# Kernel optimization log

Hardware: AMD Instinct MI355X
Metric: run time of the kernel (lower is better)

## Reference

```python
import jax, jax.numpy as jnp
import numpy as np

N, NFEAT, NHID, NCLASS, NHEADS = 4096, 512, 64, 128, 8
ALPHA = 0.2
NEG = -9e15


def leaky(x):
    return jnp.where(x > 0, x, ALPHA * x)


def setup_inputs() -> dict:
    key = jax.random.key(0)
    k = jax.random.split(key, 6)
    x = jax.random.normal(k[0], (N, NFEAT), dtype=jnp.float32)
    adj = jax.random.randint(k[1], (N, N), 0, 2, dtype=jnp.int32)
    # per-head params (xavier-ish scale)
    W = jax.random.normal(k[2], (NHEADS, NFEAT, NHID), dtype=jnp.float32) * (1.414 * (2.0 / (NFEAT + NHID)) ** 0.5)
    a = jax.random.normal(k[3], (NHEADS, 2 * NHID), dtype=jnp.float32) * (1.414 * (2.0 / (2 * NHID + 1)) ** 0.5)
    W_out = jax.random.normal(k[4], (NHEADS * NHID, NCLASS), dtype=jnp.float32) * (1.414 * (2.0 / (NHEADS * NHID + NCLASS)) ** 0.5)
    a_out = jax.random.normal(k[5], (2 * NCLASS,), dtype=jnp.float32) * (1.414 * (2.0 / (2 * NCLASS + 1)) ** 0.5)
    return {"x": x, "adj": adj, "W": W, "a": a, "W_out": W_out, "a_out": a_out}


def _gat_layer_multihead(x, adj_mask, W, a):
    # x: [N,F_in], W: [H,F_in,F_out], a: [H,2*F_out]
    h = jnp.einsum('nf,hfo->hno', x, W)           # [H,N,F_out]
    Fo = W.shape[-1]
    a1, a2 = a[:, :Fo], a[:, Fo:]                  # [H,F_out] each
    fi = jnp.einsum('hno,ho->hn', h, a1)           # score contribution of node i
    fj = jnp.einsum('hno,ho->hn', h, a2)
    e = leaky(fi[:, :, None] + fj[:, None, :])     # [H,N,N] == leakyrelu(a . [h_i||h_j])
    e = jnp.where(adj_mask[None], e, NEG)
    att = jax.nn.softmax(e, axis=-1)
    return jnp.einsum('hij,hjo->hio', att, h)      # [H,N,F_out]


def reference(x, adj, W, a, W_out, a_out):
    adj_mask = adj > 0
    # multi-head hidden layer, concat heads (dropout is identity in eval mode)
    hp = _gat_layer_multihead(x, adj_mask, W, a)            # [H,N,NHID]
    xcat = jnp.transpose(hp, (1, 0, 2)).reshape(N, NHEADS * NHID)
    # output attention layer (single head)
    out = _gat_layer_multihead(xcat, adj_mask, W_out[None], a_out[None])[0]  # [N,NCLASS]
    out = jax.nn.elu(out)
    return jax.nn.log_softmax(out, axis=1)
```

## Files before the change

### kernel.cpp

```cpp
#include <hip/hip_runtime.h>
#include <hip/hip_bf16.h>

#define NNODE 4096

typedef __attribute__((ext_vector_type(8))) short bf16x8;
typedef __attribute__((ext_vector_type(4))) float f32x4;
typedef __attribute__((ext_vector_type(8))) unsigned short us8;

__device__ __forceinline__ float leaky(float x) { return x > 0.0f ? x : 0.2f * x; }

__device__ __forceinline__ unsigned short f2bf(float x) {
  __hip_bfloat16 b = __float2bfloat16(x);
  return __builtin_bit_cast(unsigned short, b);
}

__global__ __launch_bounds__(256) void packadj(
    const int* __restrict__ adj, unsigned long long* __restrict__ mask) {
  size_t wid = (size_t)blockIdx.x * 4 + (threadIdx.x >> 6);
  int v = adj[wid * 64 + (threadIdx.x & 63)];
  unsigned long long b = __ballot(v != 0);
  if ((threadIdx.x & 63) == 0) mask[wid] = b;
}

__global__ __launch_bounds__(256) void gemm64(
    const float* __restrict__ A, const float* __restrict__ B, float* __restrict__ C,
    int M, int K, int Nfull) {
  __shared__ float Ast[64][68];
  __shared__ float Bs[64][68];
  const int t  = threadIdx.x;
  const int i0 = blockIdx.x * 64;
  const int c0 = blockIdx.y * 64;
  const int h  = blockIdx.z;
  const float* Bh = B + (size_t)h * K * Nfull;
  float*       Ch = C + (size_t)h * M * Nfull;
  const int tx = t & 15, ty = t >> 4;
  const int lrow = t >> 4;
  const int lcol = (t & 15) * 4;
  float acc[4][4] = {};

  for (int k0 = 0; k0 < K; k0 += 64) {
    #pragma unroll
    for (int s = 0; s < 4; ++s) {
      int r = lrow + s * 16;
      float4 av = *(const float4*)&A[(size_t)(i0 + r) * K + k0 + lcol];
      Ast[lcol + 0][r] = av.x;
      Ast[lcol + 1][r] = av.y;
      Ast[lcol + 2][r] = av.z;
      Ast[lcol + 3][r] = av.w;
      float4 bv = *(const float4*)&Bh[(size_t)(k0 + r) * Nfull + c0 + lcol];
      *(float4*)&Bs[r][lcol] = bv;
    }
    __syncthreads();
    #pragma unroll 8
    for (int k = 0; k < 64; ++k) {
      float4 a4 = *(const float4*)&Ast[k][ty * 4];
      float4 b4 = *(const float4*)&Bs[k][tx * 4];
      acc[0][0] += a4.x * b4.x; acc[0][1] += a4.x * b4.y; acc[0][2] += a4.x * b4.z; acc[0][3] += a4.x * b4.w;
      acc[1][0] += a4.y * b4.x; acc[1][1] += a4.y * b4.y; acc[1][2] += a4.y * b4.z; acc[1][3] += a4.y * b4.w;
      acc[2][0] += a4.z * b4.x; acc[2][1] += a4.z * b4.y; acc[2][2] += a4.z * b4.z; acc[2][3] += a4.z * b4.w;
      acc[3][0] += a4.w * b4.x; acc[3][1] += a4.w * b4.y; acc[3][2] += a4.w * b4.z; acc[3][3] += a4.w * b4.w;
    }
    __syncthreads();
  }
  #pragma unroll
  for (int mi = 0; mi < 4; ++mi) {
    #pragma unroll
    for (int ni = 0; ni < 4; ++ni)
      Ch[(size_t)(i0 + ty * 4 + mi) * Nfull + c0 + tx * 4 + ni] = acc[mi][ni];
  }
}

__global__ __launch_bounds__(256) void transpose_bf16(
    const float* __restrict__ src, short* __restrict__ dst, int Fsrc) {
  __shared__ float tile[64][68];
  const int t  = threadIdx.x;
  const int n0 = blockIdx.x * 64, o0 = blockIdx.y * 64;
  const int h  = blockIdx.z;
  const float* S = src + ((size_t)h * NNODE + n0) * Fsrc + o0;
  short* D = dst + ((size_t)h * Fsrc + o0) * NNODE + n0;
  const int r = t >> 2, cs = (t & 3) * 16;
  #pragma unroll
  for (int k2 = 0; k2 < 4; ++k2) {
    float4 v = *(const float4*)&S[(size_t)r * Fsrc + cs + k2 * 4];
    *(float4*)&tile[r][cs + k2 * 4] = v;
  }
  __syncthreads();
  const int o = t >> 2, ns = (t & 3) * 16;
  us8 u0, u1;
  #pragma unroll
  for (int e = 0; e < 8; ++e) u0[e] = f2bf(tile[ns + e][o]);
  #pragma unroll
  for (int e = 0; e < 8; ++e) u1[e] = f2bf(tile[ns + 8 + e][o]);
  *(us8*)&D[(size_t)o * NNODE + ns]     = u0;
  *(us8*)&D[(size_t)o * NNODE + ns + 8] = u1;
}

template<int F>
__global__ __launch_bounds__(256) void fifj_kernel(
    const float* __restrict__ hbuf, const float* __restrict__ avec,
    float* __restrict__ fi, float* __restrict__ fj) {
  const int gid  = blockIdx.x * 4 + (threadIdx.x >> 6);
  const int lane = threadIdx.x & 63;
  const int h = gid >> 12;
  const int n = gid & 4095;
  const float* hrow = hbuf + ((size_t)h * NNODE + n) * F;
  const float* a1 = avec + h * 2 * F;
  const float* a2 = a1 + F;
  float v1 = 0.f, v2 = 0.f;
  #pragma unroll
  for (int e = lane; e < F; e += 64) {
    float xv = hrow[e];
    v1 += xv * a1[e];
    v2 += xv * a2[e];
  }
  #pragma unroll
  for (int off = 32; off; off >>= 1) {
    v1 += __shfl_xor(v1, off);
    v2 += __shfl_xor(v2, off);
  }
  if (lane == 0) {
    fi[h * NNODE + n] = v1;
    fj[h * NNODE + n] = v2;
  }
}

template<int OT, int JLEN>
__global__ __launch_bounds__(256) void pv_split(
    const short* __restrict__ hT, const float* __restrict__ fi,
    const float* __restrict__ fj, const unsigned long long* __restrict__ mask,
    float* __restrict__ pnum, float* __restrict__ pl, int Fh) {
  __shared__ short pT[64][72];
  __shared__ short hTl[OT][64][72];
  __shared__ float fjL[64];
  __shared__ float lred[64][4];

  const int t      = threadIdx.x;
  const int lane   = t & 63;
  const int w      = t >> 6;
  const int i0     = blockIdx.x * 64;
  const int chunk  = blockIdx.y;
  const int nchunk = gridDim.y;
  const int h      = blockIdx.z;
  const int hN     = h * NNODE;
  const short* hTs = hT + (size_t)h * Fh * NNODE;

  const int R0 = (w >> 1) * 32;
  const int C0 = (w & 1) * 32;
  const int lr = lane & 15;
  const int lk = lane >> 4;

  const int ar = t >> 2;
  const int jc = (t & 3) * 16;
  const float fir = fi[hN + i0 + ar];
  const unsigned short* mrow =
      (const unsigned short*)mask + (size_t)(i0 + ar) * (NNODE / 16);

  f32x4 acc[OT][2][2] = {};
  float lsum = 0.0f;

  const int jbase = chunk * JLEN;
  for (int jt = 0; jt < JLEN; jt += 64) {
    const int j0 = jbase + jt;
    {
      const int o = t >> 2, seg = t & 3;
      #pragma unroll
      for (int ot = 0; ot < OT; ++ot) {
        const short* src = hTs + (size_t)(ot * 64 + o) * NNODE + j0 + seg * 16;
        float4 v0 = *(const float4*)(src);
        float4 v1 = *(const float4*)(src + 8);
        *(float4*)&hTl[ot][o][seg * 16]     = v0;
        *(float4*)&hTl[ot][o][seg * 16 + 8] = v1;
      }
    }
    if (t < 64) fjL[t] = fj[hN + j0 + t];
    __syncthreads();

    {
      unsigned int mb = mrow[(j0 + jc) >> 4];
      unsigned short pk[16];
      #pragma unroll
      for (int g = 0; g < 4; ++g) {
        float4 f4 = *(const float4*)&fjL[jc + g * 4];
        float s0 = fir + f4.x, s1 = fir + f4.y, s2 = fir + f4.z, s3 = fir + f4.w;
        float e0 = __expf(s0 > 0.f ? s0 : 0.2f * s0);
        float e1 = __expf(s1 > 0.f ? s1 : 0.2f * s1);
        float e2 = __expf(s2 > 0.f ? s2 : 0.2f * s2);
        float e3 = __expf(s3 > 0.f ? s3 : 0.2f * s3);
        float p0 = (mb & (1u << (4 * g + 0))) ? e0 : 0.f;
        float p1 = (mb & (1u << (4 * g + 1))) ? e1 : 0.f;
        float p2 = (mb & (1u << (4 * g + 2))) ? e2 : 0.f;
        float p3 = (mb & (1u << (4 * g + 3))) ? e3 : 0.f;
        lsum += p0 + p1 + p2 + p3;
        pk[4 * g + 0] = f2bf(p0); pk[4 * g + 1] = f2bf(p1);
        pk[4 * g + 2] = f2bf(p2); pk[4 * g + 3] = f2bf(p3);
      }
      *(us8*)&pT[ar][jc]     = *(const us8*)&pk[0];
      *(us8*)&pT[ar][jc + 8] = *(const us8*)&pk[8];
    }
    __syncthreads();

    #pragma unroll
    for (int kc = 0; kc < 64; kc += 32) {
      bf16x8 a0 = *(const bf16x8*)&pT[R0 + lr][kc + lk * 8];
      bf16x8 a1 = *(const bf16x8*)&pT[R0 + 16 + lr][kc + lk * 8];
      #pragma unroll
      for (int ot = 0; ot < OT; ++ot) {
        bf16x8 b0 = *(const bf16x8*)&hTl[ot][C0 + lr][kc + lk * 8];
        bf16x8 b1 = *(const bf16x8*)&hTl[ot][C0 + 16 + lr][kc + lk * 8];
        acc[ot][0][0] = __builtin_amdgcn_mfma_f32_16x16x32_bf16(a0, b0, acc[ot][0][0], 0, 0, 0);
        acc[ot][0][1] = __builtin_amdgcn_mfma_f32_16x16x32_bf16(a0, b1, acc[ot][0][1], 0, 0, 0);
        acc[ot][1][0] = __builtin_amdgcn_mfma_f32_16x16x32_bf16(a1, b0, acc[ot][1][0], 0, 0, 0);
        acc[ot][1][1] = __builtin_amdgcn_mfma_f32_16x16x32_bf16(a1, b1, acc[ot][1][1], 0, 0, 0);
      }
    }
    __syncthreads();
  }

  lred[ar][t & 3] = lsum;
  __syncthreads();
  if (t < 64)
    pl[(size_t)(h * nchunk + chunk) * NNODE + i0 + t] =
        lred[t][0] + lred[t][1] + lred[t][2] + lred[t][3];

  float* pout = pnum + ((size_t)(h * nchunk + chunk) * NNODE + i0) * (OT * 64);
  #pragma unroll
  for (int ot = 0; ot < OT; ++ot) {
    #pragma unroll
    for (int fa = 0; fa < 2; ++fa) {
      #pragma unroll
      for (int fb = 0; fb < 2; ++fb) {
        #pragma unroll
        for (int reg = 0; reg < 4; ++reg) {
          int row = R0 + fa * 16 + lk * 4 + reg;
          int col = ot * 64 + C0 + fb * 16 + lr;
          pout[(size_t)row * (OT * 64) + col] = acc[ot][fa][fb][reg];
        }
      }
    }
  }
}

template<int NC>
__global__ __launch_bounds__(256) void combine1(
    const float* __restrict__ pnum, const float* __restrict__ pl,
    float* __restrict__ xcat) {
  const int n = blockIdx.x, t = threadIdx.x;
  #pragma unroll
  for (int rep = 0; rep < 2; ++rep) {
    int col = t + rep * 256;
    int h = col >> 6, o = col & 63;
    float s = 0.f, L = 0.f;
    #pragma unroll
    for (int c = 0; c < NC; ++c) {
      s += pnum[((size_t)(h * NC + c) * NNODE + n) * 64 + o];
      L += pl[(size_t)(h * NC + c) * NNODE + n];
    }
    xcat[(size_t)n * 512 + col] = s / L;
  }
}

__global__ __launch_bounds__(128) void combine2_final(
    const float* __restrict__ pnum, const float* __restrict__ pl,
    float* __restrict__ dout) {
  const int n = blockIdx.x, t = threadIdx.x;
  float s = 0.f, L = 0.f;
  #pragma unroll
  for (int c = 0; c < 8; ++c) {
    s += pnum[((size_t)c * NNODE + n) * 128 + t];
    L += pl[(size_t)c * NNODE + n];
  }
  float v = s / L;
  float e = v > 0.f ? v : (__expf(v) - 1.0f);
  float mx = e;
  #pragma unroll
  for (int off = 32; off; off >>= 1) mx = fmaxf(mx, __shfl_xor(mx, off));
  __shared__ float r2[2];
  if ((t & 63) == 0) r2[t >> 6] = mx;
  __syncthreads();
  mx = fmaxf(r2[0], r2[1]);
  float sm = __expf(e - mx);
  #pragma unroll
  for (int off = 32; off; off >>= 1) sm += __shfl_xor(sm, off);
  __shared__ float s2[2];
  if ((t & 63) == 0) s2[t >> 6] = sm;
  __syncthreads();
  float sum = s2[0] + s2[1];
  dout[(size_t)n * 128 + t] = e - mx - __logf(sum);
}

extern "C" void kernel_launch(void* const* d_in, const int* in_sizes, int n_in,
                              void* d_out, int out_size, void* d_ws, size_t ws_size,
                              hipStream_t stream) {
  const float* x     = (const float*)d_in[0];
  const int*   adj   = (const int*)d_in[1];
  const float* W     = (const float*)d_in[2];
  const float* a     = (const float*)d_in[3];
  const float* W_out = (const float*)d_in[4];
  const float* a_out = (const float*)d_in[5];
  float* out = (float*)d_out;

  float* ws = (float*)d_ws;
  unsigned long long* mask = (unsigned long long*)ws;
  float* hbuf = ws + 524288;
  float* xcat = hbuf + 2097152;
  short* hT   = (short*)(xcat + 2097152);
  float* pnum = (float*)(((short*)hT) + 2097152);
  float* pl   = pnum + 4194304;
  float* fi1  = pl + 131072;
  float* fj1  = fi1 + 32768;
  float* fi2  = fj1 + 32768;
  float* fj2  = fi2 + 4096;

  packadj<<<dim3(NNODE * NNODE / 64 / 4), 256, 0, stream>>>(adj, mask);

  gemm64<<<dim3(64, 1, 8), 256, 0, stream>>>(x, W, hbuf, 4096, 512, 64);
  transpose_bf16<<<dim3(64, 1, 8), 256, 0, stream>>>(hbuf, hT, 64);
  fifj_kernel<64><<<dim3(8 * 4096 / 4), 256, 0, stream>>>(hbuf, a, fi1, fj1);
  pv_split<1, 2048><<<dim3(64, 2, 8), 256, 0, stream>>>(hT, fi1, fj1, mask, pnum, pl, 64);
  combine1<2><<<dim3(NNODE), 256, 0, stream>>>(pnum, pl, xcat);

  gemm64<<<dim3(64, 2, 1), 256, 0, stream>>>(xcat, W_out, hbuf, 4096, 512, 128);
  transpose_bf16<<<dim3(64, 2, 1), 256, 0, stream>>>(hbuf, hT, 128);
  fifj_kernel<128><<<dim3(4096 / 4), 256, 0, stream>>>(hbuf, a_out, fi2, fj2);
  pv_split<2, 512><<<dim3(64, 8, 1), 256, 0, stream>>>(hT, fi2, fj2, mask, pnum, pl, 128);
  combine2_final<<<dim3(NNODE), 128, 0, stream>>>(pnum, pl, out);
}
```

Before: 289.6 us.

## Use MFMA bf16 GEMMs, precompute W·a, and factor exp of attention scores

Replaces the scalar fp32 feature GEMMs with bf16 MFMA GEMMs that read a pre-transposed bf16 copy of the weights. Attention projections fi/fj are now computed directly from x·(W·a), using a small precomputed W·a vector, so they no longer depend on the GEMM output. The per-edge exp(leaky(fi+fj)) is factored into products of per-node exponentials chosen by a sign test, which removes the transcendental from the N×N inner loop. The cost is more small launches, lower GEMM precision, and possible overflow or precision loss when the separated exponentials are large.

```diff
diff --git a/kernel.cpp b/kernel.cpp
--- a/kernel.cpp
+++ b/kernel.cpp
@@ -6,8 +6,6 @@
 typedef __attribute__((ext_vector_type(8))) short bf16x8;
 typedef __attribute__((ext_vector_type(4))) float f32x4;
 typedef __attribute__((ext_vector_type(8))) unsigned short us8;
-
-__device__ __forceinline__ float leaky(float x) { return x > 0.0f ? x : 0.2f * x; }
 
 __device__ __forceinline__ unsigned short f2bf(float x) {
   __hip_bfloat16 b = __float2bfloat16(x);
@@ -22,62 +20,14 @@
   if ((threadIdx.x & 63) == 0) mask[wid] = b;
 }
 
-__global__ __launch_bounds__(256) void gemm64(
-    const float* __restrict__ A, const float* __restrict__ B, float* __restrict__ C,
-    int M, int K, int Nfull) {
-  __shared__ float Ast[64][68];
-  __shared__ float Bs[64][68];
-  const int t  = threadIdx.x;
-  const int i0 = blockIdx.x * 64;
-  const int c0 = blockIdx.y * 64;
-  const int h  = blockIdx.z;
-  const float* Bh = B + (size_t)h * K * Nfull;
-  float*       Ch = C + (size_t)h * M * Nfull;
-  const int tx = t & 15, ty = t >> 4;
-  const int lrow = t >> 4;
-  const int lcol = (t & 15) * 4;
-  float acc[4][4] = {};
-
-  for (int k0 = 0; k0 < K; k0 += 64) {
-    #pragma unroll
-    for (int s = 0; s < 4; ++s) {
-      int r = lrow + s * 16;
-      float4 av = *(const float4*)&A[(size_t)(i0 + r) * K + k0 + lcol];
-      Ast[lcol + 0][r] = av.x;
-      Ast[lcol + 1][r] = av.y;
-      Ast[lcol + 2][r] = av.z;
-      Ast[lcol + 3][r] = av.w;
-      float4 bv = *(const float4*)&Bh[(size_t)(k0 + r) * Nfull + c0 + lcol];
-      *(float4*)&Bs[r][lcol] = bv;
-    }
-    __syncthreads();
-    #pragma unroll 8
-    for (int k = 0; k < 64; ++k) {
-      float4 a4 = *(const float4*)&Ast[k][ty * 4];
-      float4 b4 = *(const float4*)&Bs[k][tx * 4];
-      acc[0][0] += a4.x * b4.x; acc[0][1] += a4.x * b4.y; acc[0][2] += a4.x * b4.z; acc[0][3] += a4.x * b4.w;
-      acc[1][0] += a4.y * b4.x; acc[1][1] += a4.y * b4.y; acc[1][2] += a4.y * b4.z; acc[1][3] += a4.y * b4.w;
-      acc[2][0] += a4.z * b4.x; acc[2][1] += a4.z * b4.y; acc[2][2] += a4.z * b4.z; acc[2][3] += a4.z * b4.w;
-      acc[3][0] += a4.w * b4.x; acc[3][1] += a4.w * b4.y; acc[3][2] += a4.w * b4.z; acc[3][3] += a4.w * b4.w;
-    }
-    __syncthreads();
-  }
-  #pragma unroll
-  for (int mi = 0; mi < 4; ++mi) {
-    #pragma unroll
-    for (int ni = 0; ni < 4; ++ni)
-      Ch[(size_t)(i0 + ty * 4 + mi) * Nfull + c0 + tx * 4 + ni] = acc[mi][ni];
-  }
-}
-
 __global__ __launch_bounds__(256) void transpose_bf16(
-    const float* __restrict__ src, short* __restrict__ dst, int Fsrc) {
+    const float* __restrict__ src, short* __restrict__ dst, int Nr, int Fsrc) {
   __shared__ float tile[64][68];
   const int t  = threadIdx.x;
   const int n0 = blockIdx.x * 64, o0 = blockIdx.y * 64;
   const int h  = blockIdx.z;
-  const float* S = src + ((size_t)h * NNODE + n0) * Fsrc + o0;
-  short* D = dst + ((size_t)h * Fsrc + o0) * NNODE + n0;
+  const float* S = src + ((size_t)h * Nr + n0) * Fsrc + o0;
+  short* D = dst + ((size_t)h * Fsrc + o0) * Nr + n0;
   const int r = t >> 2, cs = (t & 3) * 16;
   #pragma unroll
   for (int k2 = 0; k2 < 4; ++k2) {
@@ -91,27 +41,143 @@
   for (int e = 0; e < 8; ++e) u0[e] = f2bf(tile[ns + e][o]);
   #pragma unroll
   for (int e = 0; e < 8; ++e) u1[e] = f2bf(tile[ns + 8 + e][o]);
-  *(us8*)&D[(size_t)o * NNODE + ns]     = u0;
-  *(us8*)&D[(size_t)o * NNODE + ns + 8] = u1;
+  *(us8*)&D[(size_t)o * Nr + ns]     = u0;
+  *(us8*)&D[(size_t)o * Nr + ns + 8] = u1;
+}
+
+__global__ __launch_bounds__(256) void gemm_mfma(
+    const float* __restrict__ A, const short* __restrict__ Wt,
+    float* __restrict__ C, int M, int K, int Nfull) {
+  __shared__ short As[64][72];
+  const int t  = threadIdx.x;
+  const int lane = t & 63;
+  const int w  = t >> 6;
+  const int i0 = blockIdx.x * 64;
+  const int c0 = blockIdx.y * 64;
+  const int h  = blockIdx.z;
+  const short* Bh = Wt + ((size_t)h * Nfull + c0) * K;
+  float*       Ch = C + (size_t)h * M * Nfull;
+
+  const int R0 = (w >> 1) * 32;
+  const int C0 = (w & 1) * 32;
+  const int lr = lane & 15;
+  const int lk = lane >> 4;
+
+  const int arow = t >> 2;
+  const int aseg = (t & 3) * 16;
+
+  f32x4 acc[2][2] = {};
+
+  const short* b00p = &Bh[(size_t)(C0 + lr) * K + lk * 8];
+  const short* b10p = &Bh[(size_t)(C0 + 16 + lr) * K + lk * 8];
+
+  bf16x8 bc[4];
+  bc[0] = *(const bf16x8*)(b00p);
+  bc[1] = *(const bf16x8*)(b10p);
+  bc[2] = *(const bf16x8*)(b00p + 32);
+  bc[3] = *(const bf16x8*)(b10p + 32);
+
+  for (int k0 = 0; k0 < K; k0 += 64) {
+    {
+      const float* src = &A[(size_t)(i0 + arow) * K + k0 + aseg];
+      float4 v0 = *(const float4*)(src);
+      float4 v1 = *(const float4*)(src + 4);
+      float4 v2 = *(const float4*)(src + 8);
+      float4 v3 = *(const float4*)(src + 12);
+      us8 u0, u1;
+      u0[0] = f2bf(v0.x); u0[1] = f2bf(v0.y); u0[2] = f2bf(v0.z); u0[3] = f2bf(v0.w);
+      u0[4] = f2bf(v1.x); u0[5] = f2bf(v1.y); u0[6] = f2bf(v1.z); u0[7] = f2bf(v1.w);
+      u1[0] = f2bf(v2.x); u1[1] = f2bf(v2.y); u1[2] = f2bf(v2.z); u1[3] = f2bf(v2.w);
+      u1[4] = f2bf(v3.x); u1[5] = f2bf(v3.y); u1[6] = f2bf(v3.z); u1[7] = f2bf(v3.w);
+      *(us8*)&As[arow][aseg]     = u0;
+      *(us8*)&As[arow][aseg + 8] = u1;
+    }
+    bf16x8 bn[4];
+    {
+      int kn = (k0 + 64 < K) ? (k0 + 64) : k0;
+      bn[0] = *(const bf16x8*)(b00p + kn);
+      bn[1] = *(const bf16x8*)(b10p + kn);
+      bn[2] = *(const bf16x8*)(b00p + kn + 32);
+      bn[3] = *(const bf16x8*)(b10p + kn + 32);
+    }
+    __syncthreads();
+    #pragma unroll
+    for (int kc = 0; kc < 64; kc += 32) {
+      bf16x8 a0 = *(const bf16x8*)&As[R0 + lr][kc + lk * 8];
+      bf16x8 a1 = *(const bf16x8*)&As[R0 + 16 + lr][kc + lk * 8];
+      bf16x8 b0 = bc[(kc >> 5) * 2 + 0];
+      bf16x8 b1 = bc[(kc >> 5) * 2 + 1];
+      acc[0][0] = __builtin_amdgcn_mfma_f32_16x16x32_bf16(a0, b0, acc[0][0], 0, 0, 0);
+      acc[0][1] = __builtin_amdgcn_mfma_f32_16x16x32_bf16(a0, b1, acc[0][1], 0, 0, 0);
+      acc[1][0] = __builtin_amdgcn_mfma_f32_16x16x32_bf16(a1, b0, acc[1][0], 0, 0, 0);
+      acc[1][1] = __builtin_amdgcn_mfma_f32_16x16x32_bf16(a1, b1, acc[1][1], 0, 0, 0);
+    }
+    bc[0] = bn[0]; bc[1] = bn[1]; bc[2] = bn[2]; bc[3] = bn[3];
+    __syncthreads();
+  }
+
+  #pragma unroll
+  for (int fa = 0; fa < 2; ++fa) {
+    #pragma unroll
+    for (int fb = 0; fb < 2; ++fb) {
+      #pragma unroll
+      for (int reg = 0; reg < 4; ++reg) {
+        int row = R0 + fa * 16 + lk * 4 + reg;
+        int col = C0 + fb * 16 + lr;
+        Ch[(size_t)(i0 + row) * Nfull + c0 + col] = acc[fa][fb][reg];
+      }
+    }
+  }
 }
 
 template<int F>
-__global__ __launch_bounds__(256) void fifj_kernel(
-    const float* __restrict__ hbuf, const float* __restrict__ avec,
-    float* __restrict__ fi, float* __restrict__ fj) {
+__global__ __launch_bounds__(256) void wa_kernel(
+    const float* __restrict__ W, const float* __restrict__ a,
+    float* __restrict__ wa) {
+  const int gid  = blockIdx.x * 4 + (threadIdx.x >> 6);
+  const int lane = threadIdx.x & 63;
+  const int h = gid >> 9;
+  const int k = gid & 511;
+  const float* wrow = W + ((size_t)h * 512 + k) * F;
+  const float* ah = a + h * 2 * F;
+  float v1 = 0.f, v2 = 0.f;
+  #pragma unroll
+  for (int o = lane; o < F; o += 64) {
+    float wv = wrow[o];
+    v1 += wv * ah[o];
+    v2 += wv * ah[F + o];
+  }
+  #pragma unroll
+  for (int off = 32; off; off >>= 1) {
+    v1 += __shfl_xor(v1, off);
+    v2 += __shfl_xor(v2, off);
+  }
+  if (lane == 0) {
+    wa[((size_t)h * 2 + 0) * 512 + k] = v1;
+    wa[((size_t)h * 2 + 1) * 512 + k] = v2;
+  }
+}
+
+template<int NH>
+__global__ __launch_bounds__(256) void fidot_kernel(
+    const float* __restrict__ X, const float* __restrict__ wa,
+    float* __restrict__ fi, float* __restrict__ fj,
+    float* __restrict__ eiP, float* __restrict__ eiN,
+    float* __restrict__ ejP, float* __restrict__ ejN) {
   const int gid  = blockIdx.x * 4 + (threadIdx.x >> 6);
   const int lane = threadIdx.x & 63;
   const int h = gid >> 12;
   const int n = gid & 4095;
-  const float* hrow = hbuf + ((size_t)h * NNODE + n) * F;
-  const float* a1 = avec + h * 2 * F;
-  const float* a2 = a1 + F;
+  const float* xr = X + (size_t)n * 512;
+  const float* w1 = wa + (size_t)h * 2 * 512;
+  const float* w2 = w1 + 512;
   float v1 = 0.f, v2 = 0.f;
   #pragma unroll
-  for (int e = lane; e < F; e += 64) {
-    float xv = hrow[e];
-    v1 += xv * a1[e];
-    v2 += xv * a2[e];
+  for (int it = 0; it < 8; ++it) {
+    int k = lane + it * 64;
+    float xv = xr[k];
+    v1 += xv * w1[k];
+    v2 += xv * w2[k];
   }
   #pragma unroll
   for (int off = 32; off; off >>= 1) {
@@ -119,19 +185,26 @@
     v2 += __shfl_xor(v2, off);
   }
   if (lane == 0) {
-    fi[h * NNODE + n] = v1;
-    fj[h * NNODE + n] = v2;
+    int idx = h * NNODE + n;
+    fi[idx] = v1;
+    fj[idx] = v2;
+    eiP[idx] = __expf(v1);
+    eiN[idx] = __expf(0.2f * v1);
+    ejP[idx] = __expf(v2);
+    ejN[idx] = __expf(0.2f * v2);
   }
 }
 
 template<int OT, int JLEN>
 __global__ __launch_bounds__(256) void pv_split(
     const short* __restrict__ hT, const float* __restrict__ fi,
-    const float* __restrict__ fj, const unsigned long long* __restrict__ mask,
+    const float* __restrict__ eiP, const float* __restrict__ eiN,
+    const float* __restrict__ fj, const float* __restrict__ ejP,
+    const float* __restrict__ ejN, const unsigned long long* __restrict__ mask,
     float* __restrict__ pnum, float* __restrict__ pl, int Fh) {
   __shared__ short pT[64][72];
   __shared__ short hTl[OT][64][72];
-  __shared__ float fjL[64];
+  __shared__ float fjL[64], ejPL[64], ejNL[64];
   __shared__ float lred[64][4];
 
   const int t      = threadIdx.x;
@@ -151,7 +224,9 @@
 
   const int ar = t >> 2;
   const int jc = (t & 3) * 16;
-  const float fir = fi[hN + i0 + ar];
+  const float thr  = -fi[hN + i0 + ar];
+  const float eiPr = eiP[hN + i0 + ar];
+  const float eiNr = eiN[hN + i0 + ar];
   const unsigned short* mrow =
       (const unsigned short*)mask + (size_t)(i0 + ar) * (NNODE / 16);
 
@@ -172,7 +247,11 @@
         *(float4*)&hTl[ot][o][seg * 16 + 8] = v1;
       }
     }
-    if (t < 64) fjL[t] = fj[hN + j0 + t];
+    if (t < 64) {
+      fjL[t]  = fj[hN + j0 + t];
+      ejPL[t] = ejP[hN + j0 + t];
+      ejNL[t] = ejN[hN + j0 + t];
+    }
     __syncthreads();
 
     {
@@ -181,15 +260,16 @@
       #pragma unroll
       for (int g = 0; g < 4; ++g) {
         float4 f4 = *(const float4*)&fjL[jc + g * 4];
-        float s0 = fir + f4.x, s1 = fir + f4.y, s2 = fir + f4.z, s3 = fir + f4.w;
-        float e0 = __expf(s0 > 0.f ? s0 : 0.2f * s0);
-        float e1 = __expf(s1 > 0.f ? s1 : 0.2f * s1);
-        float e2 = __expf(s2 > 0.f ? s2 : 0.2f * s2);
-        float e3 = __expf(s3 > 0.f ? s3 : 0.2f * s3);
-        float p0 = (mb & (1u << (4 * g + 0))) ? e0 : 0.f;
-        float p1 = (mb & (1u << (4 * g + 1))) ? e1 : 0.f;
-        float p2 = (mb & (1u << (4 * g + 2))) ? e2 : 0.f;
-        float p3 = (mb & (1u << (4 * g + 3))) ? e3 : 0.f;
+        float4 eP = *(const float4*)&ejPL[jc + g * 4];
+        float4 eN = *(const float4*)&ejNL[jc + g * 4];
+        float p0 = (f4.x > thr) ? eiPr * eP.x : eiNr * eN.x;
+        float p1 = (f4.y > thr) ? eiPr * eP.y : eiNr * eN.y;
+        float p2 = (f4.z > thr) ? eiPr * eP.z : eiNr * eN.z;
+        float p3 = (f4.w > thr) ? eiPr * eP.w : eiNr * eN.w;
+        p0 = (mb & (1u << (4 * g + 0))) ? p0 : 0.f;
+        p1 = (mb & (1u << (4 * g + 1))) ? p1 : 0.f;
+        p2 = (mb & (1u << (4 * g + 2))) ? p2 : 0.f;
+        p3 = (mb & (1u << (4 * g + 3))) ? p3 : 0.f;
         lsum += p0 + p1 + p2 + p3;
         pk[4 * g + 0] = f2bf(p0); pk[4 * g + 1] = f2bf(p1);
         pk[4 * g + 2] = f2bf(p2); pk[4 * g + 3] = f2bf(p3);
@@ -306,22 +386,38 @@
   short* hT   = (short*)(xcat + 2097152);
   float* pnum = (float*)(((short*)hT) + 2097152);
   float* pl   = pnum + 4194304;
-  float* fi1  = pl + 131072;
+  short* Wt1  = (short*)(pl + 131072);
+  short* Wt2  = Wt1 + 262144;
+  float* fi1  = (float*)(Wt2 + 65536);
   float* fj1  = fi1 + 32768;
-  float* fi2  = fj1 + 32768;
+  float* eiP1 = fj1 + 32768;
+  float* eiN1 = eiP1 + 32768;
+  float* ejP1 = eiN1 + 32768;
+  float* ejN1 = ejP1 + 32768;
+  float* fi2  = ejN1 + 32768;
   float* fj2  = fi2 + 4096;
+  float* eiP2 = fj2 + 4096;
+  float* eiN2 = eiP2 + 4096;
+  float* ejP2 = eiN2 + 4096;
+  float* ejN2 = ejP2 + 4096;
+  float* wa1  = ejN2 + 4096;
+  float* wa2  = wa1 + 8192;
 
   packadj<<<dim3(NNODE * NNODE / 64 / 4), 256, 0, stream>>>(adj, mask);
-
-  gemm64<<<dim3(64, 1, 8), 256, 0, stream>>>(x, W, hbuf, 4096, 512, 64);
-  transpose_bf16<<<dim3(64, 1, 8), 256, 0, stream>>>(hbuf, hT, 64);
-  fifj_kernel<64><<<dim3(8 * 4096 / 4), 256, 0, stream>>>(hbuf, a, fi1, fj1);
-  pv_split<1, 2048><<<dim3(64, 2, 8), 256, 0, stream>>>(hT, fi1, fj1, mask, pnum, pl, 64);
+  transpose_bf16<<<dim3(8, 1, 8), 256, 0, stream>>>(W, Wt1, 512, 64);
+  transpose_bf16<<<dim3(8, 2, 1), 256, 0, stream>>>(W_out, Wt2, 512, 128);
+  wa_kernel<64><<<dim3(8 * 512 / 4), 256, 0, stream>>>(W, a, wa1);
+  wa_kernel<128><<<dim3(512 / 4), 256, 0, stream>>>(W_out, a_out, wa2);
+
+  gemm_mfma<<<dim3(64, 1, 8), 256, 0, stream>>>(x, Wt1, hbuf, 4096, 512, 64);
+  transpose_bf16<<<dim3(64, 1, 8), 256, 0, stream>>>(hbuf, hT, 4096, 64);
+  fidot_kernel<8><<<dim3(8 * 4096 / 4), 256, 0, stream>>>(x, wa1, fi1, fj1, eiP1, eiN1, ejP1, ejN1);
+  pv_split<1, 2048><<<dim3(64, 2, 8), 256, 0, stream>>>(hT, fi1, eiP1, eiN1, fj1, ejP1, ejN1, mask, pnum, pl, 64);
   combine1<2><<<dim3(NNODE), 256, 0, stream>>>(pnum, pl, xcat);
 
-  gemm64<<<dim3(64, 2, 1), 256, 0, stream>>>(xcat, W_out, hbuf, 4096, 512, 128);
-  transpose_bf16<<<dim3(64, 2, 1), 256, 0, stream>>>(hbuf, hT, 128);
-  fifj_kernel<128><<<dim3(4096 / 4), 256, 0, stream>>>(hbuf, a_out, fi2, fj2);
-  pv_split<2, 512><<<dim3(64, 8, 1), 256, 0, stream>>>(hT, fi2, fj2, mask, pnum, pl, 128);
+  gemm_mfma<<<dim3(64, 2, 1), 256, 0, stream>>>(xcat, Wt2, hbuf, 4096, 512, 128);
+  transpose_bf16<<<dim3(64, 2, 1), 256, 0, stream>>>(hbuf, hT, 4096, 128);
+  fidot_kernel<1><<<dim3(4096 / 4), 256, 0, stream>>>(xcat, wa2, fi2, fj2, eiP2, eiN2, ejP2, ejN2);
+  pv_split<2, 512><<<dim3(64, 8, 1), 256, 0, stream>>>(hT, fi2, eiP2, eiN2, fj2, ejP2, ejN2, mask, pnum, pl, 128);
   combine2_final<<<dim3(NNODE), 128, 0, stream>>>(pnum, pl, out);
 }
```

Result: faster. 273.2 us (-5.7%).
